# Kernel optimization log

Hardware: AMD Instinct MI355X
Metric: run time of the kernel (lower is better)

Reference implementation:

```python
import jax, jax.numpy as jnp
import numpy as np


def setup_inputs() -> dict:
    key = jax.random.key(0)
    ks = jax.random.split(key, 8)
    B, S, H = 2, 2048, 2048
    Hq, Hkv, D = 16, 4, H // 16
    s = 0.02
    return {
        "query": jax.random.normal(ks[0], (B, S, H), jnp.float32),
        "key": jax.random.normal(ks[1], (B, S, H), jnp.float32),
        "value": jax.random.normal(ks[2], (B, S, H), jnp.float32),
        "Wq": jax.random.normal(ks[3], (H, Hq * D), jnp.float32) * s,
        "bq": jnp.zeros((Hq * D,), jnp.float32),
        "Wk": jax.random.normal(ks[4], (H, Hkv * D), jnp.float32) * s,
        "bk": jnp.zeros((Hkv * D,), jnp.float32),
        "Wv": jax.random.normal(ks[5], (H, Hkv * D), jnp.float32) * s,
        "bv": jnp.zeros((Hkv * D,), jnp.float32),
        "Wo": jax.random.normal(ks[6], (H, H), jnp.float32) * s,
        "bo": jnp.zeros((H,), jnp.float32),
    }


def reference(query, key, value, Wq, bq, Wk, bk, Wv, bv, Wo, bo):
    Hq, Hkv = 16, 4
    B, S, H = query.shape
    D = H // Hq
    G = Hq // Hkv  # heads per KV group
    # projections
    q = query @ Wq + bq   # [B,S,Hq*D]
    k = key @ Wk + bk     # [B,S,Hkv*D]
    v = value @ Wv + bv   # [B,S,Hkv*D]
    # [B, Hkv(groups), G(heads per group), S, D] for q; [B, Hkv, S, D] for k,v
    q = q.reshape(B, S, Hkv, G, D).transpose(0, 2, 3, 1, 4)
    k = k.reshape(B, S, Hkv, D).transpose(0, 2, 1, 3)
    v = v.reshape(B, S, Hkv, D).transpose(0, 2, 1, 3)
    # NOTE: original module applies NO 1/sqrt(D) scaling -- kept faithful.
    attn = jnp.einsum('bghqd,bgkd->bghqk', q, k)  # [B,Hkv,G,S,S]
    attn = jax.nn.softmax(attn, axis=-1)
    out = jnp.einsum('bghqk,bgkd->bghqd', attn, v)  # [B,Hkv,G,S,D]
    # permute(0,3,1,2,4) -> [B,S,Hkv,G,D] -> [B,S,H]
    out = out.transpose(0, 3, 1, 2, 4).reshape(B, S, H)
    return out @ Wo + bo
```

## Files before the change

kernel.cpp:

```cpp
#include <hip/hip_runtime.h>
#include <hip/hip_bf16.h>
#include <type_traits>
#include <stdint.h>

typedef short bf16x8 __attribute__((ext_vector_type(8)));
typedef short short4v __attribute__((ext_vector_type(4)));
typedef float f32x4 __attribute__((ext_vector_type(4)));
typedef float f32x16 __attribute__((ext_vector_type(16)));

#define GLL16(gp, lp) __builtin_amdgcn_global_load_lds( \
    (const __attribute__((address_space(1))) void*)(gp), \
    (__attribute__((address_space(3))) void*)(lp), 16, 0, 0)

__device__ inline short f2bf(float f) {
    union { float f; uint32_t u; } v;
    v.f = f;
    uint32_t r = (v.u + 0x7FFFu + ((v.u >> 16) & 1u)) >> 16;
    return (short)(uint16_t)r;
}

__device__ inline bf16x8 cvt8(const float4& a, const float4& b) {
    bf16x8 o;
    o[0] = f2bf(a.x); o[1] = f2bf(a.y); o[2] = f2bf(a.z); o[3] = f2bf(a.w);
    o[4] = f2bf(b.x); o[5] = f2bf(b.y); o[6] = f2bf(b.z); o[7] = f2bf(b.w);
    return o;
}

__device__ inline uint32_t cvtpk(float lo, float hi) {
    uint32_t r;
    asm("v_cvt_pk_bf16_f32 %0, %1, %2" : "=v"(r) : "v"(lo), "v"(hi));
    return r;
}

__device__ inline bf16x8 mk8(uint32_t a, uint32_t b, uint32_t c, uint32_t d) {
    union { uint32_t u[4]; bf16x8 v; } t;
    t.u[0] = a; t.u[1] = b; t.u[2] = c; t.u[3] = d;
    return t.v;
}

__device__ inline void xchg_pf(const uint32_t c[8], bool hib, bf16x8& fA, bf16x8& fB) {
    uint32_t p0 = (uint32_t)__shfl_xor((int)c[0], 32);
    uint32_t p1 = (uint32_t)__shfl_xor((int)c[1], 32);
    uint32_t p2 = (uint32_t)__shfl_xor((int)c[2], 32);
    uint32_t p3 = (uint32_t)__shfl_xor((int)c[3], 32);
    fA = mk8(hib ? p2 : c[0], hib ? p3 : c[1], hib ? c[2] : p0, hib ? c[3] : p1);
    uint32_t p4 = (uint32_t)__shfl_xor((int)c[4], 32);
    uint32_t p5 = (uint32_t)__shfl_xor((int)c[5], 32);
    uint32_t p6 = (uint32_t)__shfl_xor((int)c[6], 32);
    uint32_t p7 = (uint32_t)__shfl_xor((int)c[7], 32);
    fB = mk8(hib ? p6 : c[4], hib ? p7 : c[5], hib ? c[6] : p4, hib ? c[7] : p5);
}

__device__ inline int probe_permlane_mode() {
#if defined(__has_builtin) && __has_builtin(__builtin_amdgcn_permlane32_swap)
    int lane = (int)(threadIdx.x & 63);
    int a = lane, b = lane + 1000;
    auto r = __builtin_amdgcn_permlane32_swap(a, b, false, false);
    int l0  = __builtin_amdgcn_readfirstlane(r[0]);
    int l32 = __builtin_amdgcn_readlane(r[0], 32);
    if (l0 == 0 && l32 == 1000) return 1;
    if (l0 == 1032 && l32 == 32) return 2;
    return 0;
#else
    return 0;
#endif
}

__global__ __launch_bounds__(256) void prep(
    const float* __restrict__ Wq, const float* __restrict__ Wk,
    const float* __restrict__ Wv, const float* __restrict__ Wo,
    short* __restrict__ WqT, short* __restrict__ WkT,
    short* __restrict__ WvT, short* __restrict__ WoT,
    const float* __restrict__ q, const float* __restrict__ k, const float* __restrict__ v,
    short* __restrict__ Xq, short* __restrict__ Xk, short* __restrict__ Xv)
{
    __shared__ short Tt[64][65];
    const int K = 2048;
    int bid = blockIdx.x;
    int t = threadIdx.x;
    if (bid < 2560) {
        const float* W; short* T; int N; int l;
        if (bid < 1024)      { W = Wq; T = WqT; N = 2048; l = bid; }
        else if (bid < 1280) { W = Wk; T = WkT; N = 512;  l = bid - 1024; }
        else if (bid < 1536) { W = Wv; T = WvT; N = 512;  l = bid - 1280; }
        else                 { W = Wo; T = WoT; N = 2048; l = bid - 1536; }
        int nt = N >> 6;
        int n0 = (l % nt) * 64, k0 = (l / nt) * 64;
        int kl = t >> 2, nb = (t & 3) * 16;
        const float* wp = W + (size_t)(k0 + kl) * N + n0 + nb;
        #pragma unroll
        for (int j = 0; j < 16; ++j) Tt[nb + j][kl] = f2bf(wp[j]);
        __syncthreads();
        int nl = t >> 2, kb = (t & 3) * 16;
        short* op = T + (size_t)(n0 + nl) * K + k0 + kb;
        #pragma unroll
        for (int j = 0; j < 16; ++j) op[j] = Tt[nl][kb + j];
    } else {
        size_t tid = (size_t)(bid - 2560) * 256 + t;
        #pragma unroll
        for (int it = 0; it < 2; ++it) {
            size_t i = tid + (size_t)it * 524288;
            const float4* p;
            p = (const float4*)(q + i * 8);
            *(bf16x8*)(Xq + i * 8) = cvt8(p[0], p[1]);
            p = (const float4*)(k + i * 8);
            *(bf16x8*)(Xk + i * 8) = cvt8(p[0], p[1]);
            p = (const float4*)(v + i * 8);
            *(bf16x8*)(Xv + i * 8) = cvt8(p[0], p[1]);
        }
    }
}

__global__ __launch_bounds__(256) void prepW(
    const float* __restrict__ Wq, const float* __restrict__ Wk,
    const float* __restrict__ Wv, const float* __restrict__ Wo,
    short* __restrict__ WqT, short* __restrict__ WkT,
    short* __restrict__ WvT, short* __restrict__ WoT)
{
    __shared__ short Tt[64][65];
    const int K = 2048;
    int bid = blockIdx.x;
    int t = threadIdx.x;
    const float* W; short* T; int N; int l;
    if (bid < 1024)      { W = Wq; T = WqT; N = 2048; l = bid; }
    else if (bid < 1280) { W = Wk; T = WkT; N = 512;  l = bid - 1024; }
    else if (bid < 1536) { W = Wv; T = WvT; N = 512;  l = bid - 1280; }
    else                 { W = Wo; T = WoT; N = 2048; l = bid - 1536; }
    int nt = N >> 6;
    int n0 = (l % nt) * 64, k0 = (l / nt) * 64;
    int kl = t >> 2, nb = (t & 3) * 16;
    const float* wp = W + (size_t)(k0 + kl) * N + n0 + nb;
    #pragma unroll
    for (int j = 0; j < 16; ++j) Tt[nb + j][kl] = f2bf(wp[j]);
    __syncthreads();
    int nl = t >> 2, kb = (t & 3) * 16;
    short* op = T + (size_t)(n0 + nl) * K + k0 + kb;
    #pragma unroll
    for (int j = 0; j < 16; ++j) op[j] = Tt[nl][kb + j];
}

__global__ __launch_bounds__(256) void cvtk(const float* __restrict__ in,
                                            short* __restrict__ out, int n8)
{
    int i = blockIdx.x * blockDim.x + threadIdx.x;
    int stride = gridDim.x * blockDim.x;
    for (; i < n8; i += stride) {
        const float4* p = (const float4*)(in + (size_t)i * 8);
        *(bf16x8*)(out + (size_t)i * 8) = cvt8(p[0], p[1]);
    }
}

__global__ __launch_bounds__(256) void transV(const short* __restrict__ Vb,
                                              short* __restrict__ Vt)
{
    __shared__ short T[64][65];
    int s0 = blockIdx.x * 64, d0 = blockIdx.y * 64, bg = blockIdx.z;
    int b = bg >> 2, g = bg & 3;
    int t = threadIdx.x;
    int sl = t >> 2, db = (t & 3) * 16;
    const short* vp = Vb + (size_t)(b * 2048 + s0 + sl) * 512 + g * 128 + d0 + db;
    #pragma unroll
    for (int j = 0; j < 16; ++j) T[db + j][sl] = vp[j];
    __syncthreads();
    int dl = t >> 2, sb = (t & 3) * 16;
    short* op = Vt + (size_t)(bg * 128 + d0 + dl) * 2048 + s0 + sb;
    #pragma unroll
    for (int j = 0; j < 16; ++j) op[j] = T[dl][sb + j];
}

template <typename TC>
__device__ __forceinline__ void gemm_core(
    const short* __restrict__ A, const short* __restrict__ BT,
    const float* __restrict__ bias, TC* __restrict__ C,
    int N, int K, int m0, int n0, short* As, short* Bs, int epi)
{
    const int t = threadIdx.x, w = t >> 6, lane = t & 63;
    const int lr = lane & 15, lg = lane >> 4;
    const int wm = (w >> 1) * 64, wn = (w & 1) * 64;
    f32x4 acc[4][4] = {};

    const int lrow = lane >> 3;
    const int lcg = (lane & 7) ^ (lrow & 7);
    const int sw = lr & 7;

    const short* abase[2]; const short* bbase[2];
    #pragma unroll
    for (int kc = 0; kc < 2; ++kc) {
        abase[kc] = &As[(wm + lr) * 64 + (((kc * 4 + lg) ^ sw) * 8)];
        bbase[kc] = &Bs[(wn + lr) * 64 + (((kc * 4 + lg) ^ sw) * 8)];
    }
    const short* asrc = A  + (size_t)(m0 + w * 32 + lrow) * K + lcg * 8;
    const short* bsrc = BT + (size_t)(n0 + w * 32 + lrow) * K + lcg * 8;
    short* adst = &As[(w * 32) * 64];
    short* bdst = &Bs[(w * 32) * 64];

    for (int kk = 0; kk < K; kk += 64) {
        __syncthreads();
        #pragma unroll
        for (int i = 0; i < 4; ++i) {
            GLL16(asrc + (size_t)i * 8 * K, adst + i * 512);
            GLL16(bsrc + (size_t)i * 8 * K, bdst + i * 512);
        }
        asrc += 64; bsrc += 64;
        __syncthreads();
        #pragma unroll
        for (int kc = 0; kc < 2; ++kc) {
            bf16x8 af[4], bfr[4];
            #pragma unroll
            for (int i = 0; i < 4; ++i) af[i] = *(const bf16x8*)(abase[kc] + i * 1024);
            #pragma unroll
            for (int j = 0; j < 4; ++j) bfr[j] = *(const bf16x8*)(bbase[kc] + j * 1024);
            #pragma unroll
            for (int i = 0; i < 4; ++i)
                #pragma unroll
                for (int j = 0; j < 4; ++j)
                    acc[i][j] = __builtin_amdgcn_mfma_f32_16x16x32_bf16(af[i], bfr[j], acc[i][j], 0, 0, 0);
        }
    }

    if constexpr (std::is_same<TC, short>::value) {
        if (epi == 1) {
            #pragma unroll
            for (int i = 0; i < 4; ++i) {
                #pragma unroll
                for (int j = 0; j < 4; ++j) {
                    int row = m0 + wm + i * 16 + lg * 4;
                    int col = n0 + wn + j * 16 + lr;
                    short4v s4;
                    #pragma unroll
                    for (int r = 0; r < 4; ++r) s4[r] = f2bf(acc[i][j][r] + bias[col]);
                    int bb = row >> 11, ss = row & 2047;
                    *(short4v*)((short*)C + ((size_t)(bb * 4 + (col >> 7)) * 128 + (col & 127)) * 2048 + ss) = s4;
                }
            }
            return;
        }
    }
    #pragma unroll
    for (int i = 0; i < 4; ++i) {
        #pragma unroll
        for (int j = 0; j < 4; ++j) {
            #pragma unroll
            for (int r = 0; r < 4; ++r) {
                int row = m0 + wm + i * 16 + lg * 4 + r;
                int col = n0 + wn + j * 16 + lr;
                float v = acc[i][j][r] + bias[col];
                if constexpr (std::is_same<TC, short>::value)
                    C[(size_t)row * N + col] = f2bf(v);
                else
                    C[(size_t)row * N + col] = v;
            }
        }
    }
}

template <typename TC>
__global__ __launch_bounds__(256) void gemm_std(
    const short* __restrict__ A, const short* __restrict__ BT,
    const float* __restrict__ bias, TC* __restrict__ C, int N, int K)
{
    __shared__ short As[128 * 64];
    __shared__ short Bs[128 * 64];
    int bid = blockIdx.x;
    int chunk = gridDim.x >> 3;
    int wg = (bid & 7) * chunk + (bid >> 3);
    int m0 = (wg & 31) * 128, n0 = (wg >> 5) * 128;
    gemm_core<TC>(A, BT, bias, C, N, K, m0, n0, As, Bs, 0);
}

__global__ __launch_bounds__(256) void gemm_qkv(
    const short* __restrict__ Xq, const short* __restrict__ Xk, const short* __restrict__ Xv,
    const short* __restrict__ WqT, const short* __restrict__ WkT, const short* __restrict__ WvT,
    const float* __restrict__ bq, const float* __restrict__ bk, const float* __restrict__ bv,
    short* __restrict__ Qb, short* __restrict__ Kb, short* __restrict__ Vt)
{
    __shared__ short As[128 * 64];
    __shared__ short Bs[128 * 64];
    int bid = blockIdx.x;
    int wg = (bid & 7) * 96 + (bid >> 3);
    const short* A; const short* BT; const float* bi; short* C; int N; int l; int epi;
    if (wg < 512)      { l = wg;       A = Xq; BT = WqT; bi = bq; C = Qb; N = 2048; epi = 0; }
    else if (wg < 640) { l = wg - 512; A = Xk; BT = WkT; bi = bk; C = Kb; N = 512;  epi = 0; }
    else               { l = wg - 640; A = Xv; BT = WvT; bi = bv; C = Vt; N = 512;  epi = 1; }
    int m0 = (l & 31) * 128, n0 = (l >> 5) * 128;
    gemm_core<short>(A, BT, bi, C, N, 2048, m0, n0, As, Bs, epi);
}

__global__ __launch_bounds__(256, 2) void attn_kernel(
    const short* __restrict__ Qb, const short* __restrict__ Kb,
    const short* __restrict__ Vt, short* __restrict__ Ob)
{
    const int S = 2048;
    __shared__ short Ks[64 * 128];
    __shared__ short Vs[128 * 64];

    int bid = blockIdx.x;
    int wg = (bid & 7) * 64 + (bid >> 3);
    const int qt = wg & 15, bh = wg >> 4;
    const int b = bh >> 4, h = bh & 15, g = h >> 2, bg = b * 4 + g;

    const int t = threadIdx.x, w = t >> 6, lane = t & 63;
    const int l5 = lane & 31, hi = lane >> 5;
    const bool hib = hi != 0;
    const int qg = b * S + qt * 128 + w * 32 + l5;
    const float C = 1.44269504089f;

    const int mode = probe_permlane_mode();

    const short* qrow = Qb + (size_t)qg * 2048 + h * 128 + hi * 8;
    bf16x8 qf[8];
    #pragma unroll
    for (int dm = 0; dm < 8; ++dm)
        qf[dm] = *(const bf16x8*)(qrow + dm * 16);

    f32x16 o[4] = {};
    float m = -1e30f, l = 0.0f;

    const int sr4 = lane >> 4, sc4 = lane & 15;
    const int sr8 = lane >> 3, sc8 = lane & 7;
    const short* ksrc[4]; const short* vsrc[4];
    #pragma unroll
    for (int i = 0; i < 4; ++i) {
        int kr = w * 16 + i * 4 + sr4;
        ksrc[i] = Kb + (size_t)(b * S + kr) * 512 + g * 128 + ((sc4 ^ (kr & 15)) * 8);
        int d = w * 32 + i * 8 + sr8;
        vsrc[i] = Vt + (size_t)(bg * 128 + d) * 2048 + ((sc8 ^ (d & 7)) * 8);
    }

    int kx[8];
    #pragma unroll
    for (int dm = 0; dm < 8; ++dm)
        kx[dm] = (((dm * 2 + hi) ^ (l5 & 15)) * 8);
    int va[4];
    #pragma unroll
    for (int j = 0; j < 4; ++j)
        va[j] = (((2 * j + hi) ^ (l5 & 7)) * 8);

    short* kd = Ks + (w * 16) * 128 + lane * 8;
    short* vd = Vs + (w * 32) * 64 + lane * 8;

    bf16x8 kreg[4], vreg[4];
    #pragma unroll
    for (int i = 0; i < 4; ++i) {
        kreg[i] = *(const bf16x8*)(ksrc[i]);
        vreg[i] = *(const bf16x8*)(vsrc[i]);
    }

    const int NT = S / 64;
    for (int ti = 0; ti < NT; ++ti) {
        __syncthreads();
        #pragma unroll
        for (int i = 0; i < 4; ++i) {
            *(bf16x8*)(kd + i * 512) = kreg[i];
            *(bf16x8*)(vd + i * 512) = vreg[i];
        }
        __syncthreads();
        if (ti + 1 < NT) {
            size_t ko = (size_t)(ti + 1) * 64 * 512;
            int vo = (ti + 1) * 64;
            #pragma unroll
            for (int i = 0; i < 4; ++i) {
                kreg[i] = *(const bf16x8*)(ksrc[i] + ko);
                vreg[i] = *(const bf16x8*)(vsrc[i] + vo);
            }
        }

        const short* KB = Ks + l5 * 128;
        f32x16 p0 = {}, p1 = {};
        __builtin_amdgcn_s_setprio(1);
        #pragma unroll
        for (int dm = 0; dm < 8; ++dm) {
            bf16x8 k0 = *(const bf16x8*)(KB + kx[dm]);
            bf16x8 k1 = *(const bf16x8*)(KB + 4096 + kx[dm]);
            p0 = __builtin_amdgcn_mfma_f32_32x32x16_bf16(k0, qf[dm], p0, 0, 0, 0);
            p1 = __builtin_amdgcn_mfma_f32_32x32x16_bf16(k1, qf[dm], p1, 0, 0, 0);
        }
        __builtin_amdgcn_s_setprio(0);

        float mx = -1e30f;
        #pragma unroll
        for (int e = 0; e < 16; ++e) mx = fmaxf(mx, fmaxf(p0[e], p1[e]));
        mx = fmaxf(mx, __shfl_xor(mx, 32));
        if (__any(mx > m)) {
            float mn = fmaxf(m, mx);
            float sf = exp2f((m - mn) * C);
            m = mn; l *= sf;
            #pragma unroll
            for (int dblk = 0; dblk < 4; ++dblk)
                #pragma unroll
                for (int e = 0; e < 16; ++e) o[dblk][e] *= sf;
        }
        float nmc = -m * C;
        #pragma unroll
        for (int e = 0; e < 16; ++e) {
            p0[e] = exp2f(fmaf(p0[e], C, nmc));
            p1[e] = exp2f(fmaf(p1[e], C, nmc));
        }
        float rs = 0.0f;
        #pragma unroll
        for (int e = 0; e < 16; ++e) rs += p0[e] + p1[e];
        rs += __shfl_xor(rs, 32);
        l += rs;

        uint32_t c0[8], c1[8];
        #pragma unroll
        for (int i = 0; i < 8; ++i) {
            c0[i] = cvtpk(p0[2 * i], p0[2 * i + 1]);
            c1[i] = cvtpk(p1[2 * i], p1[2 * i + 1]);
        }
        bf16x8 pf[4];
#if defined(__has_builtin) && __has_builtin(__builtin_amdgcn_permlane32_swap)
        if (mode == 1) {
            auto a0 = __builtin_amdgcn_permlane32_swap((int)c0[0], (int)c0[2], false, false);
            auto a1 = __builtin_amdgcn_permlane32_swap((int)c0[1], (int)c0[3], false, false);
            auto a2 = __builtin_amdgcn_permlane32_swap((int)c0[4], (int)c0[6], false, false);
            auto a3 = __builtin_amdgcn_permlane32_swap((int)c0[5], (int)c0[7], false, false);
            pf[0] = mk8((uint32_t)a0[0], (uint32_t)a1[0], (uint32_t)a0[1], (uint32_t)a1[1]);
            pf[1] = mk8((uint32_t)a2[0], (uint32_t)a3[0], (uint32_t)a2[1], (uint32_t)a3[1]);
            auto b0 = __builtin_amdgcn_permlane32_swap((int)c1[0], (int)c1[2], false, false);
            auto b1 = __builtin_amdgcn_permlane32_swap((int)c1[1], (int)c1[3], false, false);
            auto b2 = __builtin_amdgcn_permlane32_swap((int)c1[4], (int)c1[6], false, false);
            auto b3 = __builtin_amdgcn_permlane32_swap((int)c1[5], (int)c1[7], false, false);
            pf[2] = mk8((uint32_t)b0[0], (uint32_t)b1[0], (uint32_t)b0[1], (uint32_t)b1[1]);
            pf[3] = mk8((uint32_t)b2[0], (uint32_t)b3[0], (uint32_t)b2[1], (uint32_t)b3[1]);
        } else if (mode == 2) {
            auto a0 = __builtin_amdgcn_permlane32_swap((int)c0[2], (int)c0[0], false, false);
            auto a1 = __builtin_amdgcn_permlane32_swap((int)c0[3], (int)c0[1], false, false);
            auto a2 = __builtin_amdgcn_permlane32_swap((int)c0[6], (int)c0[4], false, false);
            auto a3 = __builtin_amdgcn_permlane32_swap((int)c0[7], (int)c0[5], false, false);
            pf[0] = mk8((uint32_t)a0[1], (uint32_t)a1[1], (uint32_t)a0[0], (uint32_t)a1[0]);
            pf[1] = mk8((uint32_t)a2[1], (uint32_t)a3[1], (uint32_t)a2[0], (uint32_t)a3[0]);
            auto b0 = __builtin_amdgcn_permlane32_swap((int)c1[2], (int)c1[0], false, false);
            auto b1 = __builtin_amdgcn_permlane32_swap((int)c1[3], (int)c1[1], false, false);
            auto b2 = __builtin_amdgcn_permlane32_swap((int)c1[6], (int)c1[4], false, false);
            auto b3 = __builtin_amdgcn_permlane32_swap((int)c1[7], (int)c1[5], false, false);
            pf[2] = mk8((uint32_t)b0[1], (uint32_t)b1[1], (uint32_t)b0[0], (uint32_t)b1[0]);
            pf[3] = mk8((uint32_t)b2[1], (uint32_t)b3[1], (uint32_t)b2[0], (uint32_t)b3[0]);
        } else
#endif
        {
            xchg_pf(c0, hib, pf[0], pf[1]);
            xchg_pf(c1, hib, pf[2], pf[3]);
        }

        const short* VB = Vs + l5 * 64;
        __builtin_amdgcn_s_setprio(1);
        #pragma unroll
        for (int dblk = 0; dblk < 4; ++dblk) {
            const short* vb = VB + dblk * 2048;
            #pragma unroll
            for (int j = 0; j < 4; ++j) {
                bf16x8 vf = *(const bf16x8*)(vb + va[j]);
                o[dblk] = __builtin_amdgcn_mfma_f32_32x32x16_bf16(vf, pf[j], o[dblk], 0, 0, 0);
            }
        }
        __builtin_amdgcn_s_setprio(0);
    }

    float inv = 1.0f / l;
    short* op = Ob + (size_t)qg * 2048 + h * 128 + hi * 4;
    #pragma unroll
    for (int dblk = 0; dblk < 4; ++dblk) {
        #pragma unroll
        for (int mm = 0; mm < 4; ++mm) {
            short4v s4;
            #pragma unroll
            for (int e = 0; e < 4; ++e) s4[e] = f2bf(o[dblk][mm * 4 + e] * inv);
            *(short4v*)(op + dblk * 32 + mm * 8) = s4;
        }
    }
}

extern "C" void kernel_launch(void* const* d_in, const int* in_sizes, int n_in,
                              void* d_out, int out_size, void* d_ws, size_t ws_size,
                              hipStream_t stream)
{
    const float* query = (const float*)d_in[0];
    const float* key   = (const float*)d_in[1];
    const float* value = (const float*)d_in[2];
    const float* Wq    = (const float*)d_in[3];
    const float* bq    = (const float*)d_in[4];
    const float* Wk    = (const float*)d_in[5];
    const float* bk    = (const float*)d_in[6];
    const float* Wv    = (const float*)d_in[7];
    const float* bv    = (const float*)d_in[8];
    const float* Wo    = (const float*)d_in[9];
    const float* bo    = (const float*)d_in[10];
    float* out = (float*)d_out;

    const int BS = 4096;
    char* ws = (char*)d_ws;
    dim3 blk(256);
    const size_t MB = 1048576;

    if (ws_size >= 96 * MB) {
        short* Xq  = (short*)(ws + 0);
        short* Xk  = (short*)(ws + 16 * MB);
        short* Xv  = (short*)(ws + 32 * MB);
        short* Qb  = (short*)(ws + 48 * MB);
        short* Kb  = (short*)(ws + 64 * MB);
        short* Vtg = (short*)(ws + 72 * MB);
        short* WqT = (short*)(ws + 76 * MB);
        short* WkT = (short*)(ws + 84 * MB);
        short* WvT = (short*)(ws + 86 * MB);
        short* WoT = (short*)(ws + 88 * MB);
        short* Ob  = Xq;

        prep<<<4608, blk, 0, stream>>>(Wq, Wk, Wv, Wo, WqT, WkT, WvT, WoT,
                                       query, key, value, Xq, Xk, Xv);
        gemm_qkv<<<768, blk, 0, stream>>>(Xq, Xk, Xv, WqT, WkT, WvT, bq, bk, bv, Qb, Kb, Vtg);
        attn_kernel<<<512, blk, 0, stream>>>(Qb, Kb, Vtg, Ob);
        gemm_std<float><<<512, blk, 0, stream>>>(Ob, WoT, bo, out, 2048, 2048);
    } else {
        short* Qb  = (short*)(ws + 0);
        short* Kb  = (short*)(ws + 16777216);
        short* Vb  = (short*)(ws + 20971520);
        short* Vtg = (short*)(ws + 25165824);
        short* WqT = (short*)(ws + 29360128);
        short* WkT = (short*)(ws + 37748736);
        short* WvT = (short*)(ws + 39845888);
        short* WoT = (short*)(ws + 41943040);
        short* Xbf = (short*)(ws + 50331648);

        prepW<<<2560, blk, 0, stream>>>(Wq, Wk, Wv, Wo, WqT, WkT, WvT, WoT);
        cvtk<<<2048, blk, 0, stream>>>(query, Xbf, BS * 2048 / 8);
        gemm_std<short><<<512, blk, 0, stream>>>(Xbf, WqT, bq, Qb, 2048, 2048);
        cvtk<<<2048, blk, 0, stream>>>(key, Xbf, BS * 2048 / 8);
        gemm_std<short><<<128, blk, 0, stream>>>(Xbf, WkT, bk, Kb, 512, 2048);
        cvtk<<<2048, blk, 0, stream>>>(value, Xbf, BS * 2048 / 8);
        gemm_std<short><<<128, blk, 0, stream>>>(Xbf, WvT, bv, Vb, 512, 2048);
        transV<<<dim3(32, 2, 8), blk, 0, stream>>>(Vb, Vtg);
        attn_kernel<<<512, blk, 0, stream>>>(Qb, Kb, Vtg, Xbf);
        gemm_std<float><<<512, blk, 0, stream>>>(Xbf, WoT, bo, out, 2048, 2048);
    }
}
```

Measured before the change: 256.3 us.

## Split attention KV range across two wave halves with LDS softmax merge

Doubles the attention block to 512 threads: the two halves each process half of the key/value sequence with their own LDS buffers. At the end they combine partial max, sum and output accumulators through shared memory. This halves the serial tile loop per block and raises the number of waves per CU. In exchange it adds an LDS merge epilogue with several barriers and more shared memory per block.

```diff
diff --git a/kernel.cpp b/kernel.cpp
--- a/kernel.cpp
+++ b/kernel.cpp
@@ -286,13 +286,14 @@
     gemm_core<short>(A, BT, bi, C, N, 2048, m0, n0, As, Bs, epi);
 }
 
-__global__ __launch_bounds__(256, 2) void attn_kernel(
+__global__ __launch_bounds__(512, 4) void attn_kernel(
     const short* __restrict__ Qb, const short* __restrict__ Kb,
     const short* __restrict__ Vt, short* __restrict__ Ob)
 {
     const int S = 2048;
-    __shared__ short Ks[64 * 128];
-    __shared__ short Vs[128 * 64];
+    __shared__ short Ks[2 * 64 * 128];
+    __shared__ short Vs[2 * 128 * 64];
+    __shared__ float Ml[4][64][2];
 
     int bid = blockIdx.x;
     int wg = (bid & 7) * 64 + (bid >> 3);
@@ -300,9 +301,10 @@
     const int b = bh >> 4, h = bh & 15, g = h >> 2, bg = b * 4 + g;
 
     const int t = threadIdx.x, w = t >> 6, lane = t & 63;
+    const int wq = w & 3, half = w >> 2;
     const int l5 = lane & 31, hi = lane >> 5;
     const bool hib = hi != 0;
-    const int qg = b * S + qt * 128 + w * 32 + l5;
+    const int qg = b * S + qt * 128 + wq * 32 + l5;
     const float C = 1.44269504089f;
 
     const int mode = probe_permlane_mode();
@@ -321,10 +323,10 @@
     const short* ksrc[4]; const short* vsrc[4];
     #pragma unroll
     for (int i = 0; i < 4; ++i) {
-        int kr = w * 16 + i * 4 + sr4;
-        ksrc[i] = Kb + (size_t)(b * S + kr) * 512 + g * 128 + ((sc4 ^ (kr & 15)) * 8);
-        int d = w * 32 + i * 8 + sr8;
-        vsrc[i] = Vt + (size_t)(bg * 128 + d) * 2048 + ((sc8 ^ (d & 7)) * 8);
+        int kr = wq * 16 + i * 4 + sr4;
+        ksrc[i] = Kb + (size_t)(b * S + half * 1024 + kr) * 512 + g * 128 + ((sc4 ^ (kr & 15)) * 8);
+        int d = wq * 32 + i * 8 + sr8;
+        vsrc[i] = Vt + (size_t)(bg * 128 + d) * 2048 + half * 1024 + ((sc8 ^ (d & 7)) * 8);
     }
 
     int kx[8];
@@ -336,8 +338,8 @@
     for (int j = 0; j < 4; ++j)
         va[j] = (((2 * j + hi) ^ (l5 & 7)) * 8);
 
-    short* kd = Ks + (w * 16) * 128 + lane * 8;
-    short* vd = Vs + (w * 32) * 64 + lane * 8;
+    short* kd = Ks + half * 8192 + (wq * 16) * 128 + lane * 8;
+    short* vd = Vs + half * 8192 + (wq * 32) * 64 + lane * 8;
 
     bf16x8 kreg[4], vreg[4];
     #pragma unroll
@@ -346,7 +348,7 @@
         vreg[i] = *(const bf16x8*)(vsrc[i]);
     }
 
-    const int NT = S / 64;
+    const int NT = 1024 / 64;
     for (int ti = 0; ti < NT; ++ti) {
         __syncthreads();
         #pragma unroll
@@ -365,7 +367,7 @@
             }
         }
 
-        const short* KB = Ks + l5 * 128;
+        const short* KB = Ks + half * 8192 + l5 * 128;
         f32x16 p0 = {}, p1 = {};
         __builtin_amdgcn_s_setprio(1);
         #pragma unroll
@@ -443,7 +445,7 @@
             xchg_pf(c1, hib, pf[2], pf[3]);
         }
 
-        const short* VB = Vs + l5 * 64;
+        const short* VB = Vs + half * 8192 + l5 * 64;
         __builtin_amdgcn_s_setprio(1);
         #pragma unroll
         for (int dblk = 0; dblk < 4; ++dblk) {
@@ -457,16 +459,54 @@
         __builtin_amdgcn_s_setprio(0);
     }
 
-    float inv = 1.0f / l;
-    short* op = Ob + (size_t)qg * 2048 + h * 128 + hi * 4;
-    #pragma unroll
-    for (int dblk = 0; dblk < 4; ++dblk) {
-        #pragma unroll
-        for (int mm = 0; mm < 4; ++mm) {
-            short4v s4;
-            #pragma unroll
-            for (int e = 0; e < 4; ++e) s4[e] = f2bf(o[dblk][mm * 4 + e] * inv);
-            *(short4v*)(op + dblk * 32 + mm * 8) = s4;
+    __syncthreads();
+    float* F = (float*)Ks;
+    if (half == 1) {
+        Ml[wq][lane][0] = m;
+        Ml[wq][lane][1] = l;
+        float* dst = F + wq * 2048 + lane * 32;
+        #pragma unroll
+        for (int e = 0; e < 16; ++e) { dst[e] = o[0][e]; dst[16 + e] = o[1][e]; }
+    }
+    __syncthreads();
+    float e1 = 1.0f, e2 = 0.0f, inv = 0.0f;
+    if (half == 0) {
+        float m2 = Ml[wq][lane][0], l2 = Ml[wq][lane][1];
+        float mm = fmaxf(m, m2);
+        e1 = exp2f((m - mm) * C);
+        e2 = exp2f((m2 - mm) * C);
+        inv = 1.0f / (l * e1 + l2 * e2);
+        const float* src = F + wq * 2048 + lane * 32;
+        #pragma unroll
+        for (int e = 0; e < 16; ++e) {
+            o[0][e] = o[0][e] * e1 + src[e] * e2;
+            o[1][e] = o[1][e] * e1 + src[16 + e] * e2;
+        }
+    }
+    __syncthreads();
+    if (half == 1) {
+        float* dst = F + wq * 2048 + lane * 32;
+        #pragma unroll
+        for (int e = 0; e < 16; ++e) { dst[e] = o[2][e]; dst[16 + e] = o[3][e]; }
+    }
+    __syncthreads();
+    if (half == 0) {
+        const float* src = F + wq * 2048 + lane * 32;
+        #pragma unroll
+        for (int e = 0; e < 16; ++e) {
+            o[2][e] = o[2][e] * e1 + src[e] * e2;
+            o[3][e] = o[3][e] * e1 + src[16 + e] * e2;
+        }
+        short* op = Ob + (size_t)qg * 2048 + h * 128 + hi * 4;
+        #pragma unroll
+        for (int dblk = 0; dblk < 4; ++dblk) {
+            #pragma unroll
+            for (int mm2 = 0; mm2 < 4; ++mm2) {
+                short4v s4;
+                #pragma unroll
+                for (int e = 0; e < 4; ++e) s4[e] = f2bf(o[dblk][mm2 * 4 + e] * inv);
+                *(short4v*)(op + dblk * 32 + mm2 * 8) = s4;
+            }
         }
     }
 }
@@ -509,7 +549,7 @@
         prep<<<4608, blk, 0, stream>>>(Wq, Wk, Wv, Wo, WqT, WkT, WvT, WoT,
                                        query, key, value, Xq, Xk, Xv);
         gemm_qkv<<<768, blk, 0, stream>>>(Xq, Xk, Xv, WqT, WkT, WvT, bq, bk, bv, Qb, Kb, Vtg);
-        attn_kernel<<<512, blk, 0, stream>>>(Qb, Kb, Vtg, Ob);
+        attn_kernel<<<512, dim3(512), 0, stream>>>(Qb, Kb, Vtg, Ob);
         gemm_std<float><<<512, blk, 0, stream>>>(Ob, WoT, bo, out, 2048, 2048);
     } else {
         short* Qb  = (short*)(ws + 0);
@@ -530,7 +570,7 @@
         cvtk<<<2048, blk, 0, stream>>>(value, Xbf, BS * 2048 / 8);
         gemm_std<short><<<128, blk, 0, stream>>>(Xbf, WvT, bv, Vb, 512, 2048);
         transV<<<dim3(32, 2, 8), blk, 0, stream>>>(Vb, Vtg);
-        attn_kernel<<<512, blk, 0, stream>>>(Qb, Kb, Vtg, Xbf);
+        attn_kernel<<<512, dim3(512), 0, stream>>>(Qb, Kb, Vtg, Xbf);
         gemm_std<float><<<512, blk, 0, stream>>>(Xbf, WoT, bo, out, 2048, 2048);
     }
 }
```

After: 465.5 us. 1.82x slower.
